# Performance work log

Measured on AMD Instinct MI355X. Metric: run time of the kernel, lower is better.

## Reference

```python
import jax, jax.numpy as jnp
import numpy as np

B, M, NT, V, D, H, E, S = 4, 12, 12, 10000, 64, 3, 512, 32


def setup_inputs() -> dict:
    key = jax.random.key(0)
    ks = jax.random.split(key, 16)
    def rn(k, shape, scale=0.05):
        return jax.random.normal(k, shape, dtype=jnp.float32) * scale
    return {
        "tendency": jax.random.normal(ks[0], (B, M, V), dtype=jnp.float32),
        "periodicity": jax.random.normal(ks[1], (B, NT, V), dtype=jnp.float32),
        "edges": jax.random.randint(ks[2], (H, E, S), 0, V),
        "w1": rn(ks[3], (1, D)), "b1": rn(ks[4], (D,)),
        "w2": rn(ks[5], (D, D)), "b2": rn(ks[6], (D,)),
        "attn_w": rn(ks[7], (D, D)), "attn_a": rn(ks[8], (2 * D, 1)),
        "w_ih": rn(ks[9], (4 * D, D)), "w_hh": rn(ks[10], (4 * D, D)),
        "b_ih": rn(ks[11], (4 * D,)), "b_hh": rn(ks[12], (4 * D,)),
        "w_out": rn(ks[13], (2 * D, 1)), "b_out": rn(ks[14], (1,)),
    }


def _hypersage(X, edges, w, b):
    # X: (N, V, F); edges: (E, S) node indices. All edges have size S <= Q,
    # so torch's random subsampling is the identity.
    n, v, f = X.shape
    e, s = edges.shape
    gathered = X[:, edges, :]                      # (N, E, S, F)
    agg = gathered.mean(axis=2)                    # (N, E, F)
    flat = edges.reshape(-1)                       # (E*S,)
    contrib = jnp.broadcast_to(agg[:, :, None, :], (n, e, s, f)).reshape(n, e * s, f)
    X_out = jnp.zeros((n, v, f), X.dtype).at[:, flat, :].add(contrib)
    deg = jnp.zeros((v,), X.dtype).at[flat].add(1.0)
    deg = jnp.maximum(deg, 1.0)
    X_out = X_out / deg[None, :, None]
    return X_out @ w + b                           # Linear fc


def _attention(Xs, attn_w, attn_a):
    # Xs: (H, N, V, D)
    ref = Xs.mean(axis=0)                          # (N, V, D)
    wx = Xs @ attn_w                               # (H, N, V, D)
    wr = ref @ attn_w                              # (N, V, D)
    z = jnp.concatenate([wx, jnp.broadcast_to(wr[None], wx.shape)], axis=-1) @ attn_a
    z = jax.nn.leaky_relu(z, negative_slope=0.2)   # (H, N, V, 1)
    alpha = jax.nn.softmax(z, axis=0)
    return (alpha * Xs).sum(axis=0)                # (N, V, D)


def _lstm_final(x, w_ih, w_hh, b_ih, b_hh):
    # x: (BV, T, D) -> final hidden state (BV, D). PyTorch gate order i,f,g,o.
    bv, t, d = x.shape
    xg = x @ w_ih.T + (b_ih + b_hh)                # precompute input gates (BV, T, 4D)
    def step(carry, xg_t):
        h, c = carry
        g = xg_t + h @ w_hh.T
        i, f, gg, o = jnp.split(g, 4, axis=-1)
        c = jax.nn.sigmoid(f) * c + jax.nn.sigmoid(i) * jnp.tanh(gg)
        h = jax.nn.sigmoid(o) * jnp.tanh(c)
        return (h, c), None
    h0 = jnp.zeros((bv, d), x.dtype)
    (h, _), _ = jax.lax.scan(step, (h0, h0), jnp.swapaxes(xg, 0, 1))
    return h


def _branch(seq, edges, w1, b1, w2, b2, attn_w, attn_a, w_ih, w_hh, b_ih, b_hh):
    b, t, v = seq.shape
    X = seq.reshape(b * t, v, 1)                   # fold time into batch (same DAMHG per step)
    def per_hg(e):
        return _hypersage(_hypersage(X, e, w1, b1), e, w2, b2)
    xs = jax.vmap(per_hg)(edges)                   # (H, B*T, V, D)
    fused = _attention(xs, attn_w, attn_a)         # (B*T, V, D)
    d = fused.shape[-1]
    seq_v = fused.reshape(b, t, v, d).transpose(0, 2, 1, 3).reshape(b * v, t, d)
    h = _lstm_final(seq_v, w_ih, w_hh, b_ih, b_hh)
    return h.reshape(b, v, d)


def reference(tendency, periodicity, edges, w1, b1, w2, b2, attn_w, attn_a, w_ih, w_hh, b_ih, b_hh, w_out, b_out):
    h_t = _branch(tendency, edges, w1, b1, w2, b2, attn_w, attn_a, w_ih, w_hh, b_ih, b_hh)
    h_p = _branch(periodicity, edges, w1, b1, w2, b2, attn_w, attn_a, w_ih, w_hh, b_ih, b_hh)
    fusion = jnp.concatenate([h_t, h_p], axis=-1)  # (B, V, 2D)
    out = fusion @ w_out + b_out                   # (B, V, 1)
    return out[..., 0]
```

## Files before the change

kernel.cpp:

```cpp
#include <hip/hip_runtime.h>

#define NV 10000
#define NB 4
#define NTT 12
#define NSEQ 48
#define NH 3
#define NE 512
#define NS 32
#define ND 64

#define S_U   0
#define S_C1  64
#define S_V1  128
#define S_V2  192
#define S_SC  256
#define S_GU  272
#define S_GC  528
#define S_G0  784
#define F_INV 1040
#define F_M   (F_INV + NH*NV)
#define F_PQ  (F_M + NH*NV)
#define F_HT  (F_PQ + 4*NV*NSEQ)
#define I_CNT (F_HT + 2*NB*NV)
#define I_CUR (I_CNT + NH*NV)
#define I_OFF (I_CUR + NH*NV)
#define I_SLOT (I_OFF + NH*NV)
#define F_DYN (I_SLOT + NH*NE*NS)
#define XT_SZ  (NV*NSEQ)
#define AGG_SZ (NH*NE*NSEQ)
#define YZ_SZ  (NH*NV*NSEQ)

typedef __attribute__((ext_vector_type(8))) _Float16 f16x8;
typedef __attribute__((ext_vector_type(4))) float f32x4;

__device__ __forceinline__ unsigned short f2h(float x) {
  union { _Float16 h; unsigned short u; } c;
  c.h = (_Float16)x;
  return c.u;
}
__device__ __forceinline__ f16x8 ldsH(const unsigned short* p) {
  union { uint4 u; f16x8 v; } x;
  x.u = *(const uint4*)p;
  return x.v;
}

__global__ void k_prep(const float* __restrict__ w1, const float* __restrict__ b1,
                       const float* __restrict__ w2, const float* __restrict__ b2,
                       const float* __restrict__ attn_w, const float* __restrict__ attn_a,
                       const float* __restrict__ w_ih, const float* __restrict__ b_ih,
                       const float* __restrict__ b_hh, float* __restrict__ ws) {
  __shared__ float u_s[64], c1_s[64];
  const int tid = threadIdx.x;
  if (tid < 64) {
    float v1 = 0.f, v2 = 0.f, u = 0.f, c1 = 0.f;
    for (int d = 0; d < 64; ++d) {
      const float aw = attn_w[tid * 64 + d];
      v1 += aw * attn_a[d];
      v2 += aw * attn_a[64 + d];
      const float w2v = w2[d * 64 + tid];
      u  += w1[d] * w2v;
      c1 += b1[d] * w2v;
    }
    ws[S_U + tid] = u;  ws[S_C1 + tid] = c1;
    ws[S_V1 + tid] = v1; ws[S_V2 + tid] = v2;
    u_s[tid] = u; c1_s[tid] = c1;
  }
  __syncthreads();
  if (tid == 0) {
    float al = 0.f, be = 0.f, ga = 0.f, de = 0.f, ep = 0.f;
    for (int d = 0; d < 64; ++d) {
      const float v1 = ws[S_V1 + d], v2 = ws[S_V2 + d];
      al += u_s[d] * v1;  be += c1_s[d] * v1;
      ga += u_s[d] * v2;  de += c1_s[d] * v2;
      ep += b2[d] * (v1 + v2);
    }
    ws[S_SC + 0] = al; ws[S_SC + 1] = be; ws[S_SC + 2] = ga;
    ws[S_SC + 3] = de; ws[S_SC + 4] = ep;
  }
  {
    const int j = tid;
    float gu = 0.f, gc = 0.f, g0 = 0.f;
    for (int d = 0; d < 64; ++d) {
      const float w = w_ih[j * 64 + d];
      gu += w * u_s[d]; gc += w * c1_s[d]; g0 += w * b2[d];
    }
    ws[S_GU + j] = gu; ws[S_GC + j] = gc;
    ws[S_G0 + j] = g0 + b_ih[j] + b_hh[j];
  }
}

__global__ void k_zero(int* __restrict__ p, int n) {
  const int g = blockIdx.x * 256 + threadIdx.x;
  if (g < n) p[g] = 0;
}

__global__ void k_count(const int* __restrict__ edges, int* __restrict__ counts) {
  const int g = blockIdx.x * 256 + threadIdx.x;
  if (g >= NH * NE * NS) return;
  const int h = g >> 14;
  atomicAdd(&counts[h * NV + edges[g]], 1);
}

__global__ void k_scan(const int* __restrict__ counts, int* __restrict__ offs,
                       float* __restrict__ invdeg, float* __restrict__ mvec) {
  const int h = blockIdx.x;
  const int tid = threadIdx.x;
  const int base = h * NV;
  const int CH = 10;
  int local[10];
  int run = 0;
  for (int i = 0; i < CH; ++i) {
    const int v = tid * CH + i;
    const int c = (v < NV) ? counts[base + v] : 0;
    local[i] = run; run += c;
  }
  __shared__ int sd[1024];
  sd[tid] = run;
  __syncthreads();
  int acc = run;
  for (int off = 1; off < 1024; off <<= 1) {
    const int t = (tid >= off) ? sd[tid - off] : 0;
    __syncthreads();
    acc += t; sd[tid] = acc;
    __syncthreads();
  }
  const int excl = acc - run;
  for (int i = 0; i < CH; ++i) {
    const int v = tid * CH + i;
    if (v < NV) {
      offs[base + v] = excl + local[i];
      const int c = counts[base + v];
      invdeg[base + v] = 1.0f / (float)((c > 0) ? c : 1);
      mvec[base + v] = (c > 0) ? 1.0f : 0.0f;
    }
  }
}

__global__ void k_fill(const int* __restrict__ edges, const int* __restrict__ offs,
                       int* __restrict__ cursor, int* __restrict__ slot_edge) {
  const int g = blockIdx.x * 256 + threadIdx.x;
  if (g >= NH * NE * NS) return;
  const int h = g >> 14;
  const int e = (g >> 5) & (NE - 1);
  const int v = edges[g];
  const int pos = atomicAdd(&cursor[h * NV + v], 1);
  slot_edge[h * NE * NS + offs[h * NV + v] + pos] = e;
}

__global__ void k_trans2(const float* __restrict__ s0, const float* __restrict__ s1,
                         float* __restrict__ xT, int xtS) {
  __shared__ float tile[128][49];
  const float* seq = blockIdx.y ? s1 : s0;
  float* o = xT + (size_t)blockIdx.y * xtS;
  const int v0 = blockIdx.x * 128;
  const int tid = threadIdx.x;
  for (int i = tid; i < 128 * NSEQ; i += 256) {
    const int n = i / 128, vl = i % 128;
    const int v = v0 + vl;
    tile[vl][n] = (v < NV) ? seq[n * NV + v] : 0.0f;
  }
  __syncthreads();
  for (int i = tid; i < 128 * NSEQ; i += 256) {
    const int vl = i / NSEQ, n = i % NSEQ;
    const int v = v0 + vl;
    if (v < NV) o[v * NSEQ + n] = tile[vl][n];
  }
}

__global__ void k_eagg1(const int* __restrict__ edges, const float* __restrict__ xT,
                        int xtS, float* __restrict__ agg, int aggS) {
  const int g = blockIdx.x * 256 + threadIdx.x;
  if (g >= NH * NE * 12) return;
  const float* x = xT + (size_t)blockIdx.y * xtS;
  float* a = agg + (size_t)blockIdx.y * aggS;
  const int n0 = (g % 12) * 4;
  const int e = (g / 12) % NE;
  const int h = g / (12 * NE);
  const int* ep = edges + (h * NE + e) * NS;
  float4 acc = make_float4(0.f, 0.f, 0.f, 0.f);
  for (int s = 0; s < NS; ++s) {
    const float4 t = *(const float4*)&x[ep[s] * NSEQ + n0];
    acc.x += t.x; acc.y += t.y; acc.z += t.z; acc.w += t.w;
  }
  acc.x *= (1.0f / NS); acc.y *= (1.0f / NS); acc.z *= (1.0f / NS); acc.w *= (1.0f / NS);
  *(float4*)&a[(h * NE + e) * NSEQ + n0] = acc;
}

__global__ void k_eagg2(const int* __restrict__ edges, const float* __restrict__ ysum,
                        int yS, const float* __restrict__ invdeg,
                        float* __restrict__ agg, int aggS) {
  const int g = blockIdx.x * 256 + threadIdx.x;
  if (g >= NH * NE * 12) return;
  const float* y = ysum + (size_t)blockIdx.y * yS;
  float* a = agg + (size_t)blockIdx.y * aggS;
  const int n0 = (g % 12) * 4;
  const int e = (g / 12) % NE;
  const int h = g / (12 * NE);
  const int* ep = edges + (h * NE + e) * NS;
  float4 acc = make_float4(0.f, 0.f, 0.f, 0.f);
  for (int s = 0; s < NS; ++s) {
    const int v = ep[s];
    const float iv = invdeg[h * NV + v];
    const float4 t = *(const float4*)&y[(h * NV + v) * NSEQ + n0];
    acc.x += t.x * iv; acc.y += t.y * iv; acc.z += t.z * iv; acc.w += t.w * iv;
  }
  acc.x *= (1.0f / NS); acc.y *= (1.0f / NS); acc.z *= (1.0f / NS); acc.w *= (1.0f / NS);
  *(float4*)&a[(h * NE + e) * NSEQ + n0] = acc;
}

__global__ void k_vg(const int* __restrict__ counts, const int* __restrict__ offs,
                     const int* __restrict__ slot_edge, const float* __restrict__ agg,
                     int aggS, float* __restrict__ outv, int outS) {
  const int g = blockIdx.x * 256 + threadIdx.x;
  if (g >= NH * NV * 12) return;
  const float* a = agg + (size_t)blockIdx.y * aggS;
  float* o = outv + (size_t)blockIdx.y * outS;
  const int n0 = (g % 12) * 4;
  const int v = (g / 12) % NV;
  const int h = g / (12 * NV);
  const int beg = offs[h * NV + v];
  const int cnt = counts[h * NV + v];
  const int* se = slot_edge + h * NE * NS;
  float4 acc = make_float4(0.f, 0.f, 0.f, 0.f);
  for (int i = 0; i < cnt; ++i) {
    const int e = se[beg + i];
    const float4 t = *(const float4*)&a[(h * NE + e) * NSEQ + n0];
    acc.x += t.x; acc.y += t.y; acc.z += t.z; acc.w += t.w;
  }
  *(float4*)&o[(h * NV + v) * NSEQ + n0] = acc;
}

__global__ void k_vgattn(const int* __restrict__ counts, const int* __restrict__ offs,
                         const int* __restrict__ slot_edge, const float* __restrict__ agg,
                         int aggS, const float* __restrict__ invdeg,
                         const float* __restrict__ mvec, const float* __restrict__ ws,
                         unsigned int* __restrict__ pq, int br0) {
  const int g = blockIdx.x * 256 + threadIdx.x;
  if (g >= NV * 12) return;
  const int bi = blockIdx.y;
  const float* a = agg + (size_t)bi * aggS;
  unsigned int* pbuf = pq + (size_t)(bi + br0) * NV * NSEQ;
  const int n0 = (g % 12) * 4;
  const int v = g / 12;
  const float al = ws[S_SC + 0], be = ws[S_SC + 1], ga = ws[S_SC + 2],
              de = ws[S_SC + 3], ep = ws[S_SC + 4];
  union { float4 v4; float f[4]; } zh[3];
  float mh[3];
  #pragma unroll
  for (int h = 0; h < NH; ++h) {
    const int beg = offs[h * NV + v];
    const int cnt = counts[h * NV + v];
    const int* se = slot_edge + h * NE * NS;
    float4 acc = make_float4(0.f, 0.f, 0.f, 0.f);
    for (int i = 0; i < cnt; ++i) {
      const int e = se[beg + i];
      const float4 t = *(const float4*)&a[(h * NE + e) * NSEQ + n0];
      acc.x += t.x; acc.y += t.y; acc.z += t.z; acc.w += t.w;
    }
    const float iv = invdeg[h * NV + v];
    zh[h].v4 = make_float4(acc.x * iv, acc.y * iv, acc.z * iv, acc.w * iv);
    mh[h] = mvec[h * NV + v];
  }
  const float mb = (mh[0] + mh[1] + mh[2]) * (1.f / 3.f);
  uint4 o4;
  unsigned int* op = (unsigned int*)&o4;
  #pragma unroll
  for (int j = 0; j < 4; ++j) {
    const float z0 = zh[0].f[j], z1 = zh[1].f[j], z2 = zh[2].f[j];
    const float zb = (z0 + z1 + z2) * (1.f / 3.f);
    float sc[3];
    const float zt[3] = {z0, z1, z2};
    #pragma unroll
    for (int h = 0; h < NH; ++h) {
      const float s = al * zt[h] + be * mh[h] + ga * zb + de * mb + ep;
      sc[h] = (s > 0.f) ? s : 0.2f * s;
    }
    const float mx = fmaxf(sc[0], fmaxf(sc[1], sc[2]));
    const float e0 = __expf(sc[0] - mx), e1 = __expf(sc[1] - mx), e2 = __expf(sc[2] - mx);
    const float inv = 1.0f / (e0 + e1 + e2);
    const float pv = (e0 * z0 + e1 * z1 + e2 * z2) * inv;
    const float qv = (e0 * mh[0] + e1 * mh[1] + e2 * mh[2]) * inv;
    op[j] = (unsigned int)f2h(pv) | ((unsigned int)f2h(qv) << 16);
  }
  *(uint4*)&pbuf[v * NSEQ + n0] = o4;
}

#define RS2 72
__launch_bounds__(256, 3)
__global__ void k_lstm2(const float* __restrict__ w_hh, const float* __restrict__ ws,
                        const unsigned int* __restrict__ pqbase,
                        const float* __restrict__ w_out, float* __restrict__ part) {
  __shared__ __align__(16) unsigned short smem[4 * 64 * RS2];
  __shared__ unsigned int pq_sh[2][NTT][64];
  const int tid = threadIdx.x;
  const int w = tid >> 6, lane = tid & 63, q = lane >> 4, l15 = lane & 15;
  const int b0 = blockIdx.y * 2, br = blockIdx.z;
  const int v0 = blockIdx.x * 64;
  const int d = w * 16 + l15;

  union HU { uint4 u; f16x8 v; };

  const unsigned int* pqb = pqbase + (size_t)br * NV * NSEQ;
  for (int i = tid; i < 384; i += 256) {
    const int u = i / 192, ii = i % 192;
    const int s = ii / 3, f4 = ii % 3;
    const int v = v0 + s;
    uint4 val = make_uint4(0u, 0u, 0u, 0u);
    if (v < NV) val = *(const uint4*)&pqb[v * NSEQ + (b0 + u) * NTT + f4 * 4];
    pq_sh[u][f4 * 4 + 0][s] = val.x; pq_sh[u][f4 * 4 + 1][s] = val.y;
    pq_sh[u][f4 * 4 + 2][s] = val.z; pq_sh[u][f4 * 4 + 3][s] = val.w;
  }

  f16x8 Bf[4][2];
  #pragma unroll
  for (int g = 0; g < 4; ++g)
    #pragma unroll
    for (int kh = 0; kh < 2; ++kh) {
      const float* wp = w_hh + (g * 64 + d) * 64 + kh * 32 + q * 8;
      const float4 lo = *(const float4*)wp;
      const float4 hi = *(const float4*)(wp + 4);
      HU f;
      f.u.x = (unsigned int)f2h(lo.x) | ((unsigned int)f2h(lo.y) << 16);
      f.u.y = (unsigned int)f2h(lo.z) | ((unsigned int)f2h(lo.w) << 16);
      f.u.z = (unsigned int)f2h(hi.x) | ((unsigned int)f2h(hi.y) << 16);
      f.u.w = (unsigned int)f2h(hi.z) | ((unsigned int)f2h(hi.w) << 16);
      Bf[g][kh] = f.v;
    }

  HU bex[4];
  #pragma unroll
  for (int g = 0; g < 4; ++g) {
    const float gu = ws[S_GU + g * 64 + d];
    const float gc = ws[S_GC + g * 64 + d];
    const float g0 = ws[S_G0 + g * 64 + d];
    bex[g].u.x = (q == 0) ? ((unsigned int)f2h(gu) | ((unsigned int)f2h(gc) << 16)) : 0u;
    bex[g].u.y = (q == 0) ? (unsigned int)f2h(g0) : 0u;
    bex[g].u.z = 0u; bex[g].u.w = 0u;
  }
  const float WO = w_out[br * 64 + d];
  __syncthreads();

  f32x4 cst[2][4];
  float pr[2][4][4];
  #pragma unroll
  for (int u = 0; u < 2; ++u)
    #pragma unroll
    for (int mi = 0; mi < 4; ++mi) cst[u][mi] = (f32x4){0.f, 0.f, 0.f, 0.f};
  const f32x4 z4 = (f32x4){0.f, 0.f, 0.f, 0.f};

  #pragma unroll 1
  for (int t = 0; t < NTT; ++t) {
    const bool last = (t == NTT - 1);
    #pragma unroll
    for (int u = 0; u < 2; ++u) {
      const unsigned short* hr = smem + (u * 2 + ((t + 1) & 1)) * (64 * RS2);
      unsigned short* hw = smem + (u * 2 + (t & 1)) * (64 * RS2);
      #pragma unroll
      for (int mi = 0; mi < 4; ++mi) {
        HU ae;
        ae.u.x = (q == 0) ? pq_sh[u][t][mi * 16 + l15] : 0u;
        ae.u.y = (q == 0) ? 0x3C00u : 0u;
        ae.u.z = 0u; ae.u.w = 0u;
        f32x4 aI = __builtin_amdgcn_mfma_f32_16x16x32_f16(ae.v, bex[0].v, z4, 0, 0, 0);
        f32x4 aF = __builtin_amdgcn_mfma_f32_16x16x32_f16(ae.v, bex[1].v, z4, 0, 0, 0);
        f32x4 aG = __builtin_amdgcn_mfma_f32_16x16x32_f16(ae.v, bex[2].v, z4, 0, 0, 0);
        f32x4 aO = __builtin_amdgcn_mfma_f32_16x16x32_f16(ae.v, bex[3].v, z4, 0, 0, 0);
        if (t > 0) {
          #pragma unroll
          for (int kh = 0; kh < 2; ++kh) {
            const f16x8 Ah = ldsH(&hr[(mi * 16 + l15) * RS2 + kh * 32 + q * 8]);
            aI = __builtin_amdgcn_mfma_f32_16x16x32_f16(Ah, Bf[0][kh], aI, 0, 0, 0);
            aF = __builtin_amdgcn_mfma_f32_16x16x32_f16(Ah, Bf[1][kh], aF, 0, 0, 0);
            aG = __builtin_amdgcn_mfma_f32_16x16x32_f16(Ah, Bf[2][kh], aG, 0, 0, 0);
            aO = __builtin_amdgcn_mfma_f32_16x16x32_f16(Ah, Bf[3][kh], aO, 0, 0, 0);
          }
        }
        #pragma unroll
        for (int r = 0; r < 4; ++r) {
          const float c  = cst[u][mi][r];
          const float ea = __expf(-aI[r]);
          const float eb = __expf(-2.0f * aG[r]);
          const float ef = __expf(-aF[r]);
          const float A  = 1.0f + ea, Bb = 1.0f + eb, Fd = 1.0f + ef;
          const float P  = A * Bb;
          const float numer = fmaf(c, P, (1.0f - eb) * Fd);
          const float cn = numer * __builtin_amdgcn_rcpf(Fd * P);
          cst[u][mi][r] = cn;
          const float ec = __expf(-aO[r]);
          const float ed = __expf(-2.0f * cn);
          const float h = (1.0f - ed) *
              __builtin_amdgcn_rcpf((1.0f + ec) * (1.0f + ed));
          if (!last) {
            hw[(mi * 16 + q * 4 + r) * RS2 + d] = f2h(h);
          } else {
            pr[u][mi][r] = h * WO;
          }
        }
      }
    }
    __syncthreads();
  }
  float* fbuf = (float*)smem;
  #pragma unroll
  for (int u = 0; u < 2; ++u)
    #pragma unroll
    for (int mi = 0; mi < 4; ++mi)
      #pragma unroll
      for (int r = 0; r < 4; ++r) {
        float v = pr[u][mi][r];
        v += __shfl_xor(v, 1);
        v += __shfl_xor(v, 2);
        v += __shfl_xor(v, 4);
        v += __shfl_xor(v, 8);
        if (l15 == 0) fbuf[u * 256 + w * 64 + mi * 16 + q * 4 + r] = v;
      }
  __syncthreads();
  if (tid < 128) {
    const int u = tid >> 6, s = tid & 63;
    const int v = v0 + s;
    if (v < NV) {
      const float* fb = fbuf + u * 256;
      part[(br * NB + (b0 + u)) * NV + v] = fb[s] + fb[64 + s] + fb[128 + s] + fb[192 + s];
    }
  }
}

__global__ void k_comb(const float* __restrict__ part, const float* __restrict__ b_out,
                       float* __restrict__ out) {
  const int g = blockIdx.x * 256 + threadIdx.x;
  if (g >= NB * NV / 4) return;
  const float4 a = ((const float4*)part)[g];
  const float4 c = ((const float4*)part)[NB * NV / 4 + g];
  const float bo = b_out[0];
  float4 o;
  o.x = a.x + c.x + bo; o.y = a.y + c.y + bo;
  o.z = a.z + c.z + bo; o.w = a.w + c.w + bo;
  ((float4*)out)[g] = o;
}

extern "C" void kernel_launch(void* const* d_in, const int* in_sizes, int n_in,
                              void* d_out, int out_size, void* d_ws, size_t ws_size,
                              hipStream_t stream) {
  const float* tend   = (const float*)d_in[0];
  const float* peri   = (const float*)d_in[1];
  const int*   edges  = (const int*)d_in[2];
  const float* w1     = (const float*)d_in[3];
  const float* b1     = (const float*)d_in[4];
  const float* w2     = (const float*)d_in[5];
  const float* b2     = (const float*)d_in[6];
  const float* attn_w = (const float*)d_in[7];
  const float* attn_a = (const float*)d_in[8];
  const float* w_ih   = (const float*)d_in[9];
  const float* w_hh   = (const float*)d_in[10];
  const float* b_ih   = (const float*)d_in[11];
  const float* b_hh   = (const float*)d_in[12];
  const float* w_out  = (const float*)d_in[13];
  const float* b_out  = (const float*)d_in[14];
  float* out = (float*)d_out;
  float* ws  = (float*)d_ws;
  int*   iws = (int*)d_ws;
  int* cnt = iws + I_CNT;
  int* cur = iws + I_CUR;
  int* off = iws + I_OFF;
  int* sed = iws + I_SLOT;
  unsigned int* pqw = (unsigned int*)(ws + F_PQ);

  const size_t need2 = ((size_t)F_DYN + 2 * (XT_SZ + AGG_SZ + YZ_SZ)) * 4;
  const bool batched = ws_size >= need2;
  const int nb = batched ? 2 : 1;
  float* XT  = ws + F_DYN;
  float* AGG = XT + (size_t)nb * XT_SZ;
  float* YZ  = AGG + (size_t)nb * AGG_SZ;

  k_prep<<<1, 256, 0, stream>>>(w1, b1, w2, b2, attn_w, attn_a, w_ih, b_ih, b_hh, ws);
  k_zero<<<(2 * NH * NV + 255) / 256, 256, 0, stream>>>(cnt, 2 * NH * NV);
  k_count<<<(NH * NE * NS) / 256, 256, 0, stream>>>(edges, cnt);
  k_scan<<<NH, 1024, 0, stream>>>(cnt, off, ws + F_INV, ws + F_M);
  k_fill<<<(NH * NE * NS) / 256, 256, 0, stream>>>(edges, off, cur, sed);

  const int g_eagg = (NH * NE * 12 + 255) / 256;
  const int g_vg   = (NH * NV * 12 + 255) / 256;
  const int g_attn = (NV * 12 + 255) / 256;
  if (batched) {
    k_trans2<<<dim3((NV + 127) / 128, 2), 256, 0, stream>>>(tend, peri, XT, XT_SZ);
    k_eagg1<<<dim3(g_eagg, 2), 256, 0, stream>>>(edges, XT, XT_SZ, AGG, AGG_SZ);
    k_vg<<<dim3(g_vg, 2), 256, 0, stream>>>(cnt, off, sed, AGG, AGG_SZ, YZ, YZ_SZ);
    k_eagg2<<<dim3(g_eagg, 2), 256, 0, stream>>>(edges, YZ, YZ_SZ, ws + F_INV, AGG, AGG_SZ);
    k_vgattn<<<dim3(g_attn, 2), 256, 0, stream>>>(cnt, off, sed, AGG, AGG_SZ,
                                                  ws + F_INV, ws + F_M, ws, pqw, 0);
  } else {
    for (int br = 0; br < 2; ++br) {
      const float* seq = br ? peri : tend;
      k_trans2<<<dim3((NV + 127) / 128, 1), 256, 0, stream>>>(seq, seq, XT, 0);
      k_eagg1<<<dim3(g_eagg, 1), 256, 0, stream>>>(edges, XT, 0, AGG, 0);
      k_vg<<<dim3(g_vg, 1), 256, 0, stream>>>(cnt, off, sed, AGG, 0, YZ, 0);
      k_eagg2<<<dim3(g_eagg, 1), 256, 0, stream>>>(edges, YZ, 0, ws + F_INV, AGG, 0);
      k_vgattn<<<dim3(g_attn, 1), 256, 0, stream>>>(cnt, off, sed, AGG, 0,
                                                    ws + F_INV, ws + F_M, ws, pqw, br);
    }
  }
  dim3 lgrid((NV + 63) / 64, NB / 2, 2);
  k_lstm2<<<lgrid, 256, 0, stream>>>(w_hh, ws, pqw, w_out, ws + F_HT);
  k_comb<<<(NB * NV / 4 + 255) / 256, 256, 0, stream>>>(ws + F_HT, b_out, out);
}
```

Baseline: 265.5 us.

## Fuse zeroing into prep kernel, split LSTM per batch, atomically combine branches

Merges the zero-fill kernel into the prep kernel, which now also zeroes the output buffer. The LSTM kernel now handles one batch element per block instead of two, which halves its shared memory and register use and raises the occupancy target from 3 to 4 blocks. The final combine kernel is removed: each branch adds its partial output directly into the output with atomicAdd, and bias is added once by branch 0. This saves two launches and a pass over an intermediate buffer, but it doubles the LSTM grid, reloads weights per block, and makes the summation order of the two branches nondeterministic.

After: 242.9 us. -8.5%, faster.

```diff
diff --git a/kernel.cpp b/kernel.cpp
--- a/kernel.cpp
+++ b/kernel.cpp
@@ -30,6 +30,8 @@
 #define AGG_SZ (NH*NE*NSEQ)
 #define YZ_SZ  (NH*NV*NSEQ)
 
+#define NZERO (2*NH*NV + NB*NV)
+
 typedef __attribute__((ext_vector_type(8))) _Float16 f16x8;
 typedef __attribute__((ext_vector_type(4))) float f32x4;
 
@@ -44,13 +46,20 @@
   return x.v;
 }
 
-__global__ void k_prep(const float* __restrict__ w1, const float* __restrict__ b1,
+__global__ void k_init(const float* __restrict__ w1, const float* __restrict__ b1,
                        const float* __restrict__ w2, const float* __restrict__ b2,
                        const float* __restrict__ attn_w, const float* __restrict__ attn_a,
                        const float* __restrict__ w_ih, const float* __restrict__ b_ih,
-                       const float* __restrict__ b_hh, float* __restrict__ ws) {
+                       const float* __restrict__ b_hh, float* __restrict__ ws,
+                       int* __restrict__ cnt, float* __restrict__ out) {
+  const int tid = threadIdx.x;
+  if (blockIdx.x != 0) {
+    const int g = (blockIdx.x - 1) * 256 + tid;
+    if (g < 2 * NH * NV) cnt[g] = 0;
+    else if (g < NZERO) out[g - 2 * NH * NV] = 0.0f;
+    return;
+  }
   __shared__ float u_s[64], c1_s[64];
-  const int tid = threadIdx.x;
   if (tid < 64) {
     float v1 = 0.f, v2 = 0.f, u = 0.f, c1 = 0.f;
     for (int d = 0; d < 64; ++d) {
@@ -87,11 +96,6 @@
     ws[S_GU + j] = gu; ws[S_GC + j] = gc;
     ws[S_G0 + j] = g0 + b_ih[j] + b_hh[j];
   }
-}
-
-__global__ void k_zero(int* __restrict__ p, int n) {
-  const int g = blockIdx.x * 256 + threadIdx.x;
-  if (g < n) p[g] = 0;
 }
 
 __global__ void k_count(const int* __restrict__ edges, int* __restrict__ counts) {
@@ -286,29 +290,29 @@
 }
 
 #define RS2 72
-__launch_bounds__(256, 3)
+__launch_bounds__(256, 4)
 __global__ void k_lstm2(const float* __restrict__ w_hh, const float* __restrict__ ws,
                         const unsigned int* __restrict__ pqbase,
-                        const float* __restrict__ w_out, float* __restrict__ part) {
-  __shared__ __align__(16) unsigned short smem[4 * 64 * RS2];
-  __shared__ unsigned int pq_sh[2][NTT][64];
+                        const float* __restrict__ w_out, const float* __restrict__ b_out,
+                        float* __restrict__ out) {
+  __shared__ __align__(16) unsigned short smem[2 * 64 * RS2];
+  __shared__ unsigned int pq_sh[NTT][64];
   const int tid = threadIdx.x;
   const int w = tid >> 6, lane = tid & 63, q = lane >> 4, l15 = lane & 15;
-  const int b0 = blockIdx.y * 2, br = blockIdx.z;
+  const int b = blockIdx.y, br = blockIdx.z;
   const int v0 = blockIdx.x * 64;
   const int d = w * 16 + l15;
 
   union HU { uint4 u; f16x8 v; };
 
   const unsigned int* pqb = pqbase + (size_t)br * NV * NSEQ;
-  for (int i = tid; i < 384; i += 256) {
-    const int u = i / 192, ii = i % 192;
-    const int s = ii / 3, f4 = ii % 3;
+  if (tid < 192) {
+    const int s = tid / 3, f4 = tid % 3;
     const int v = v0 + s;
     uint4 val = make_uint4(0u, 0u, 0u, 0u);
-    if (v < NV) val = *(const uint4*)&pqb[v * NSEQ + (b0 + u) * NTT + f4 * 4];
-    pq_sh[u][f4 * 4 + 0][s] = val.x; pq_sh[u][f4 * 4 + 1][s] = val.y;
-    pq_sh[u][f4 * 4 + 2][s] = val.z; pq_sh[u][f4 * 4 + 3][s] = val.w;
+    if (v < NV) val = *(const uint4*)&pqb[v * NSEQ + b * NTT + f4 * 4];
+    pq_sh[f4 * 4 + 0][s] = val.x; pq_sh[f4 * 4 + 1][s] = val.y;
+    pq_sh[f4 * 4 + 2][s] = val.z; pq_sh[f4 * 4 + 3][s] = val.w;
   }
 
   f16x8 Bf[4][2];
@@ -338,104 +342,84 @@
     bex[g].u.z = 0u; bex[g].u.w = 0u;
   }
   const float WO = w_out[br * 64 + d];
+  const float BO = b_out[0];
   __syncthreads();
 
-  f32x4 cst[2][4];
-  float pr[2][4][4];
-  #pragma unroll
-  for (int u = 0; u < 2; ++u)
-    #pragma unroll
-    for (int mi = 0; mi < 4; ++mi) cst[u][mi] = (f32x4){0.f, 0.f, 0.f, 0.f};
+  f32x4 cst[4];
+  float pr[4][4];
+  #pragma unroll
+  for (int mi = 0; mi < 4; ++mi) cst[mi] = (f32x4){0.f, 0.f, 0.f, 0.f};
   const f32x4 z4 = (f32x4){0.f, 0.f, 0.f, 0.f};
 
   #pragma unroll 1
   for (int t = 0; t < NTT; ++t) {
+    const unsigned short* hr = smem + ((t + 1) & 1) * (64 * RS2);
+    unsigned short* hw = smem + (t & 1) * (64 * RS2);
     const bool last = (t == NTT - 1);
     #pragma unroll
-    for (int u = 0; u < 2; ++u) {
-      const unsigned short* hr = smem + (u * 2 + ((t + 1) & 1)) * (64 * RS2);
-      unsigned short* hw = smem + (u * 2 + (t & 1)) * (64 * RS2);
-      #pragma unroll
-      for (int mi = 0; mi < 4; ++mi) {
-        HU ae;
-        ae.u.x = (q == 0) ? pq_sh[u][t][mi * 16 + l15] : 0u;
-        ae.u.y = (q == 0) ? 0x3C00u : 0u;
-        ae.u.z = 0u; ae.u.w = 0u;
-        f32x4 aI = __builtin_amdgcn_mfma_f32_16x16x32_f16(ae.v, bex[0].v, z4, 0, 0, 0);
-        f32x4 aF = __builtin_amdgcn_mfma_f32_16x16x32_f16(ae.v, bex[1].v, z4, 0, 0, 0);
-        f32x4 aG = __builtin_amdgcn_mfma_f32_16x16x32_f16(ae.v, bex[2].v, z4, 0, 0, 0);
-        f32x4 aO = __builtin_amdgcn_mfma_f32_16x16x32_f16(ae.v, bex[3].v, z4, 0, 0, 0);
-        if (t > 0) {
-          #pragma unroll
-          for (int kh = 0; kh < 2; ++kh) {
-            const f16x8 Ah = ldsH(&hr[(mi * 16 + l15) * RS2 + kh * 32 + q * 8]);
-            aI = __builtin_amdgcn_mfma_f32_16x16x32_f16(Ah, Bf[0][kh], aI, 0, 0, 0);
-            aF = __builtin_amdgcn_mfma_f32_16x16x32_f16(Ah, Bf[1][kh], aF, 0, 0, 0);
-            aG = __builtin_amdgcn_mfma_f32_16x16x32_f16(Ah, Bf[2][kh], aG, 0, 0, 0);
-            aO = __builtin_amdgcn_mfma_f32_16x16x32_f16(Ah, Bf[3][kh], aO, 0, 0, 0);
-          }
-        }
+    for (int mi = 0; mi < 4; ++mi) {
+      HU ae;
+      ae.u.x = (q == 0) ? pq_sh[t][mi * 16 + l15] : 0u;
+      ae.u.y = (q == 0) ? 0x3C00u : 0u;
+      ae.u.z = 0u; ae.u.w = 0u;
+      f32x4 aI = __builtin_amdgcn_mfma_f32_16x16x32_f16(ae.v, bex[0].v, z4, 0, 0, 0);
+      f32x4 aF = __builtin_amdgcn_mfma_f32_16x16x32_f16(ae.v, bex[1].v, z4, 0, 0, 0);
+      f32x4 aG = __builtin_amdgcn_mfma_f32_16x16x32_f16(ae.v, bex[2].v, z4, 0, 0, 0);
+      f32x4 aO = __builtin_amdgcn_mfma_f32_16x16x32_f16(ae.v, bex[3].v, z4, 0, 0, 0);
+      if (t > 0) {
         #pragma unroll
-        for (int r = 0; r < 4; ++r) {
-          const float c  = cst[u][mi][r];
-          const float ea = __expf(-aI[r]);
-          const float eb = __expf(-2.0f * aG[r]);
-          const float ef = __expf(-aF[r]);
-          const float A  = 1.0f + ea, Bb = 1.0f + eb, Fd = 1.0f + ef;
-          const float P  = A * Bb;
-          const float numer = fmaf(c, P, (1.0f - eb) * Fd);
-          const float cn = numer * __builtin_amdgcn_rcpf(Fd * P);
-          cst[u][mi][r] = cn;
-          const float ec = __expf(-aO[r]);
-          const float ed = __expf(-2.0f * cn);
-          const float h = (1.0f - ed) *
-              __builtin_amdgcn_rcpf((1.0f + ec) * (1.0f + ed));
-          if (!last) {
-            hw[(mi * 16 + q * 4 + r) * RS2 + d] = f2h(h);
-          } else {
-            pr[u][mi][r] = h * WO;
-          }
+        for (int kh = 0; kh < 2; ++kh) {
+          const f16x8 Ah = ldsH(&hr[(mi * 16 + l15) * RS2 + kh * 32 + q * 8]);
+          aI = __builtin_amdgcn_mfma_f32_16x16x32_f16(Ah, Bf[0][kh], aI, 0, 0, 0);
+          aF = __builtin_amdgcn_mfma_f32_16x16x32_f16(Ah, Bf[1][kh], aF, 0, 0, 0);
+          aG = __builtin_amdgcn_mfma_f32_16x16x32_f16(Ah, Bf[2][kh], aG, 0, 0, 0);
+          aO = __builtin_amdgcn_mfma_f32_16x16x32_f16(Ah, Bf[3][kh], aO, 0, 0, 0);
         }
       }
-    }
-    __syncthreads();
-  }
-  float* fbuf = (float*)smem;
-  #pragma unroll
-  for (int u = 0; u < 2; ++u)
-    #pragma unroll
-    for (int mi = 0; mi < 4; ++mi)
       #pragma unroll
       for (int r = 0; r < 4; ++r) {
-        float v = pr[u][mi][r];
-        v += __shfl_xor(v, 1);
-        v += __shfl_xor(v, 2);
-        v += __shfl_xor(v, 4);
-        v += __shfl_xor(v, 8);
-        if (l15 == 0) fbuf[u * 256 + w * 64 + mi * 16 + q * 4 + r] = v;
+        const float c  = cst[mi][r];
+        const float ea = __expf(-aI[r]);
+        const float eb = __expf(-2.0f * aG[r]);
+        const float ef = __expf(-aF[r]);
+        const float A  = 1.0f + ea, Bb = 1.0f + eb, Fd = 1.0f + ef;
+        const float P  = A * Bb;
+        const float numer = fmaf(c, P, (1.0f - eb) * Fd);
+        const float cn = numer * __builtin_amdgcn_rcpf(Fd * P);
+        cst[mi][r] = cn;
+        const float ec = __expf(-aO[r]);
+        const float ed = __expf(-2.0f * cn);
+        const float h = (1.0f - ed) *
+            __builtin_amdgcn_rcpf((1.0f + ec) * (1.0f + ed));
+        if (!last) {
+          hw[(mi * 16 + q * 4 + r) * RS2 + d] = f2h(h);
+        } else {
+          pr[mi][r] = h * WO;
+        }
       }
+    }
+    __syncthreads();
+  }
+  float* fbuf = (float*)smem;
+  #pragma unroll
+  for (int mi = 0; mi < 4; ++mi)
+    #pragma unroll
+    for (int r = 0; r < 4; ++r) {
+      float v = pr[mi][r];
+      v += __shfl_xor(v, 1);
+      v += __shfl_xor(v, 2);
+      v += __shfl_xor(v, 4);
+      v += __shfl_xor(v, 8);
+      if (l15 == 0) fbuf[w * 64 + mi * 16 + q * 4 + r] = v;
+    }
   __syncthreads();
-  if (tid < 128) {
-    const int u = tid >> 6, s = tid & 63;
-    const int v = v0 + s;
+  if (tid < 64) {
+    const int v = v0 + tid;
     if (v < NV) {
-      const float* fb = fbuf + u * 256;
-      part[(br * NB + (b0 + u)) * NV + v] = fb[s] + fb[64 + s] + fb[128 + s] + fb[192 + s];
-    }
-  }
-}
-
-__global__ void k_comb(const float* __restrict__ part, const float* __restrict__ b_out,
-                       float* __restrict__ out) {
-  const int g = blockIdx.x * 256 + threadIdx.x;
-  if (g >= NB * NV / 4) return;
-  const float4 a = ((const float4*)part)[g];
-  const float4 c = ((const float4*)part)[NB * NV / 4 + g];
-  const float bo = b_out[0];
-  float4 o;
-  o.x = a.x + c.x + bo; o.y = a.y + c.y + bo;
-  o.z = a.z + c.z + bo; o.w = a.w + c.w + bo;
-  ((float4*)out)[g] = o;
+      const float s = fbuf[tid] + fbuf[64 + tid] + fbuf[128 + tid] + fbuf[192 + tid];
+      atomicAdd(&out[b * NV + v], s + ((br == 0) ? BO : 0.0f));
+    }
+  }
 }
 
 extern "C" void kernel_launch(void* const* d_in, const int* in_sizes, int n_in,
@@ -472,8 +456,8 @@
   float* AGG = XT + (size_t)nb * XT_SZ;
   float* YZ  = AGG + (size_t)nb * AGG_SZ;
 
-  k_prep<<<1, 256, 0, stream>>>(w1, b1, w2, b2, attn_w, attn_a, w_ih, b_ih, b_hh, ws);
-  k_zero<<<(2 * NH * NV + 255) / 256, 256, 0, stream>>>(cnt, 2 * NH * NV);
+  k_init<<<1 + (NZERO + 255) / 256, 256, 0, stream>>>(
+      w1, b1, w2, b2, attn_w, attn_a, w_ih, b_ih, b_hh, ws, cnt, out);
   k_count<<<(NH * NE * NS) / 256, 256, 0, stream>>>(edges, cnt);
   k_scan<<<NH, 1024, 0, stream>>>(cnt, off, ws + F_INV, ws + F_M);
   k_fill<<<(NH * NE * NS) / 256, 256, 0, stream>>>(edges, off, cur, sed);
@@ -499,7 +483,6 @@
                                                     ws + F_INV, ws + F_M, ws, pqw, br);
     }
   }
-  dim3 lgrid((NV + 63) / 64, NB / 2, 2);
-  k_lstm2<<<lgrid, 256, 0, stream>>>(w_hh, ws, pqw, w_out, ws + F_HT);
-  k_comb<<<(NB * NV / 4 + 255) / 256, 256, 0, stream>>>(ws + F_HT, b_out, out);
-}
+  dim3 lgrid((NV + 63) / 64, NB, 2);
+  k_lstm2<<<lgrid, 256, 0, stream>>>(w_hh, ws, pqw, w_out, b_out, out);
+}
```
